# Kernel optimization log

Hardware: AMD Instinct MI355X
Metric: run time of the kernel (lower is better)

## Reference

```python
import jax, jax.numpy as jnp
import numpy as np

EPS = 1e-5  # InstanceNorm2d default eps


def setup_inputs() -> dict:
    key = jax.random.key(0)
    ks = jax.random.split(key, 5)
    B, T, C, N, H = 4, 8, 256, 196, 4
    s = 1.0 / np.sqrt(C)
    return {
        "emb": jax.random.normal(ks[0], (B, T, C, N), dtype=jnp.float32),
        "Wq": jax.random.normal(ks[1], (H, C, C), dtype=jnp.float32) * s,
        "Wk": jax.random.normal(ks[2], (H, C, C), dtype=jnp.float32) * s,
        "Wv": jax.random.normal(ks[3], (H, C, C), dtype=jnp.float32) * s,
        "Wo": jax.random.normal(ks[4], (C, C), dtype=jnp.float32) * s,
    }


def reference(emb, Wq, Wk, Wv, Wo):
    B, T, C, N = emb.shape
    S = T * N  # KV_size
    # emb.permute(0,1,3,2).view(B, T*N, C)
    x = jnp.transpose(emb, (0, 1, 3, 2)).reshape(B, S, C)
    # per-head full-width Linear projections (nn.Linear: y = x @ W.T)
    Q = jnp.einsum("bsc,hdc->bhsd", x, Wq)  # [B,H,S,C]
    K = jnp.einsum("bsc,hdc->bhsd", x, Wk)
    V = jnp.einsum("bsc,hdc->bhsd", x, Wv)
    scores = jnp.einsum("bhsd,bhtd->bhst", Q, K) / jnp.sqrt(jnp.float32(S))
    # InstanceNorm2d over each [S,S] map per (batch, head), no affine, biased var
    mean = jnp.mean(scores, axis=(-2, -1), keepdims=True)
    var = jnp.var(scores, axis=(-2, -1), keepdims=True)
    normed = (scores - mean) * jax.lax.rsqrt(var + EPS)
    probs = jax.nn.softmax(normed, axis=-1)  # attn_dropout: eval-mode identity
    ctx = jnp.einsum("bhst,bhtd->bhsd", probs, V)  # [B,H,S,C]
    ctx = jnp.mean(ctx, axis=1)  # mean over heads -> [B,S,C]
    O1 = jnp.einsum("bsc,dc->bsd", ctx, Wo)  # out Linear; proj_dropout identity
    # .view(-1, num_frames, num_channels, num_patches) on contiguous [B, T*N, C]
    return O1.reshape(B, T, C, N)
```

## Files before the change

kernel.cpp:

```cpp
#include <hip/hip_runtime.h>
#include <stdint.h>

typedef unsigned short u16;

#define Bb 4
#define Hh 4
#define Tt 8
#define Cc 256
#define NP 196
#define Ss 1568
#define SCALE_S 0.0252538136f

typedef __attribute__((ext_vector_type(4))) float floatx4;
typedef __attribute__((ext_vector_type(8))) short shortx8;

__device__ __forceinline__ float bf2f(u16 u) {
    union { unsigned u; float f; } v; v.u = ((unsigned)u) << 16; return v.f;
}
__device__ __forceinline__ u16 f2bf(float f) {
    union { float f; unsigned u; } v; v.f = f;
    unsigned r = v.u + 0x7FFFu + ((v.u >> 16) & 1u);
    return (u16)(r >> 16);
}

__global__ __launch_bounds__(256) void k_convw(const float* __restrict__ src, u16* __restrict__ dst, int n) {
    int i = blockIdx.x * 256 + threadIdx.x;
    if (i < n) dst[i] = f2bf(src[i]);
}

__device__ __forceinline__ void mfma_step(const u16* As, const u16* Bs, int lane,
                                          int wm, int wn, floatx4 acc[4][4]) {
    const int r15 = lane & 15;
    const int kq  = (lane >> 4) << 3;
    shortx8 a[4], b[4];
#pragma unroll
    for (int i = 0; i < 4; ++i)
        a[i] = *(const shortx8*)(As + (wm * 64 + i * 16 + r15) * 32 + kq);
#pragma unroll
    for (int j = 0; j < 4; ++j)
        b[j] = *(const shortx8*)(Bs + (wn * 64 + j * 16 + r15) * 32 + kq);
#pragma unroll
    for (int i = 0; i < 4; ++i)
#pragma unroll
        for (int j = 0; j < 4; ++j)
            acc[i][j] = __builtin_amdgcn_mfma_f32_16x16x32_bf16(a[i], b[j], acc[i][j], 0, 0, 0);
}

__device__ __forceinline__ void gemm_bt_core(const u16* A, const u16* Bm, int lda, int ldb,
                                             int mbase, int mlast, int nbase, int nlast,
                                             int KD, u16* As, u16* Bs, floatx4 acc[4][4]) {
    int tid = threadIdx.x;
    int lane = tid & 63, wave = tid >> 6, wm = wave >> 1, wn = wave & 1;
    int row0 = tid >> 2, row1 = 64 + (tid >> 2);
    int cole = (tid & 3) << 3;
    int ga0 = mbase + row0; ga0 = ga0 <= mlast ? ga0 : mlast;
    int ga1 = mbase + row1; ga1 = ga1 <= mlast ? ga1 : mlast;
    int gb0 = nbase + row0; gb0 = gb0 <= nlast ? gb0 : nlast;
    int gb1 = nbase + row1; gb1 = gb1 <= nlast ? gb1 : nlast;
    const u16* pa0 = A  + (size_t)ga0 * lda + cole;
    const u16* pa1 = A  + (size_t)ga1 * lda + cole;
    const u16* pb0 = Bm + (size_t)gb0 * ldb + cole;
    const u16* pb1 = Bm + (size_t)gb1 * ldb + cole;
    shortx8 va0 = *(const shortx8*)(pa0);
    shortx8 va1 = *(const shortx8*)(pa1);
    shortx8 vb0 = *(const shortx8*)(pb0);
    shortx8 vb1 = *(const shortx8*)(pb1);
    for (int k0 = 0; k0 < KD; k0 += 32) {
        __syncthreads();
        *(shortx8*)(As + row0 * 32 + cole) = va0;
        *(shortx8*)(As + row1 * 32 + cole) = va1;
        *(shortx8*)(Bs + row0 * 32 + cole) = vb0;
        *(shortx8*)(Bs + row1 * 32 + cole) = vb1;
        int k1 = k0 + 32;
        if (k1 < KD) {
            va0 = *(const shortx8*)(pa0 + k1);
            va1 = *(const shortx8*)(pa1 + k1);
            vb0 = *(const shortx8*)(pb0 + k1);
            vb1 = *(const shortx8*)(pb1 + k1);
        }
        __syncthreads();
        mfma_step(As, Bs, lane, wm, wn, acc);
    }
}

__global__ void k_transpose(const float* __restrict__ emb, u16* __restrict__ x) {
    __shared__ u16 tile[32][33];
    int bt = blockIdx.z;
    int c0 = blockIdx.y * 32, n0 = blockIdx.x * 32;
    const float* src = emb + (size_t)bt * Cc * NP;
#pragma unroll
    for (int rr = 0; rr < 32; rr += 8) {
        int c = c0 + threadIdx.y + rr;
        int n = n0 + threadIdx.x;
        u16 v = 0;
        if (n < NP) v = f2bf(src[(size_t)c * NP + n]);
        tile[threadIdx.y + rr][threadIdx.x] = v;
    }
    __syncthreads();
    int b = bt / Tt, t = bt % Tt;
    u16* dst = x + ((size_t)b * Ss + (size_t)t * NP) * Cc;
#pragma unroll
    for (int rr = 0; rr < 32; rr += 8) {
        int n = n0 + threadIdx.y + rr;
        int c = c0 + threadIdx.x;
        if (n < NP) dst[(size_t)n * Cc + c] = tile[threadIdx.x][threadIdx.y + rr];
    }
}

__global__ __launch_bounds__(256) void k_qkv(const u16* __restrict__ x,
                                             const u16* __restrict__ Wq,
                                             const u16* __restrict__ Wk,
                                             const u16* __restrict__ Wv,
                                             u16* __restrict__ Q, u16* __restrict__ Kb,
                                             u16* __restrict__ Vt) {
    __shared__ __align__(16) u16 As[128 * 32], Bs[128 * 32];
    floatx4 acc[4][4];
#pragma unroll
    for (int i = 0; i < 4; ++i)
#pragma unroll
        for (int j = 0; j < 4; ++j) acc[i][j] = (floatx4)(0.f);
    int z = blockIdx.z;
    int qkv = z >> 4, bh = z & 15, b = bh >> 2, h = bh & 3;
    const u16* A = x + (size_t)b * Ss * Cc;
    const u16* W = (qkv == 0 ? Wq : (qkv == 1 ? Wk : Wv)) + (size_t)h * Cc * Cc;
    int mbase = blockIdx.y * 128, nbase = blockIdx.x * 128;
    gemm_bt_core(A, W, Cc, Cc, mbase, Ss - 1, nbase, Cc - 1, Cc, As, Bs, acc);

    int tid = threadIdx.x, lane = tid & 63, wave = tid >> 6, wm = wave >> 1, wn = wave & 1;
    int rq = (lane >> 4) << 2, cn = lane & 15;
    if (qkv < 2) {
        u16* out = (qkv == 0 ? Q : Kb) + (size_t)bh * Ss * Cc;
#pragma unroll
        for (int i = 0; i < 4; ++i) {
            int mb = mbase + wm * 64 + i * 16 + rq;
#pragma unroll
            for (int j = 0; j < 4; ++j) {
                int n = nbase + wn * 64 + j * 16 + cn;
#pragma unroll
                for (int r = 0; r < 4; ++r) {
                    int m = mb + r;
                    if (m < Ss) out[(size_t)m * Cc + n] = f2bf(acc[i][j][r]);
                }
            }
        }
    } else {
        u16* out = Vt + (size_t)bh * Cc * Ss;
#pragma unroll
        for (int i = 0; i < 4; ++i) {
            int m0 = mbase + wm * 64 + i * 16 + rq;
            if (m0 < Ss) {
#pragma unroll
                for (int j = 0; j < 4; ++j) {
                    int n = nbase + wn * 64 + j * 16 + cn;
                    ushort4 v;
                    v.x = f2bf(acc[i][j][0]); v.y = f2bf(acc[i][j][1]);
                    v.z = f2bf(acc[i][j][2]); v.w = f2bf(acc[i][j][3]);
                    *(ushort4*)(out + (size_t)n * Ss + m0) = v;
                }
            }
        }
    }
}

__global__ __launch_bounds__(256) void k_scores(const u16* __restrict__ Q,
                                                const u16* __restrict__ Kb,
                                                u16* __restrict__ Sc, float* __restrict__ stats) {
    __shared__ __align__(16) u16 As[128 * 32], Bs[128 * 32];
    __shared__ float sred[8];
    floatx4 acc[4][4];
#pragma unroll
    for (int i = 0; i < 4; ++i)
#pragma unroll
        for (int j = 0; j < 4; ++j) acc[i][j] = (floatx4)(0.f);
    int bh = blockIdx.z;
    const u16* A  = Q  + (size_t)bh * Ss * Cc;
    const u16* Bm = Kb + (size_t)bh * Ss * Cc;
    int mbase = blockIdx.y * 128, nbase = blockIdx.x * 128;
    gemm_bt_core(A, Bm, Cc, Cc, mbase, Ss - 1, nbase, Ss - 1, Cc, As, Bs, acc);

    int tid = threadIdx.x, lane = tid & 63, wave = tid >> 6, wm = wave >> 1, wn = wave & 1;
    int rq = (lane >> 4) << 2, cn = lane & 15;
    u16* out = Sc + (size_t)bh * Ss * Ss;
    float lsum = 0.f, lsq = 0.f;
#pragma unroll
    for (int i = 0; i < 4; ++i) {
        int mb = mbase + wm * 64 + i * 16 + rq;
#pragma unroll
        for (int j = 0; j < 4; ++j) {
            int n = nbase + wn * 64 + j * 16 + cn;
            bool nv = n < Ss;
#pragma unroll
            for (int r = 0; r < 4; ++r) {
                int m = mb + r;
                if (nv && m < Ss) {
                    float v = acc[i][j][r] * SCALE_S;
                    out[(size_t)m * Ss + n] = f2bf(v);
                    lsum += v; lsq += v * v;
                }
            }
        }
    }
#pragma unroll
    for (int mk = 1; mk <= 32; mk <<= 1) { lsum += __shfl_xor(lsum, mk); lsq += __shfl_xor(lsq, mk); }
    if (lane == 0) { sred[wave] = lsum; sred[4 + wave] = lsq; }
    __syncthreads();
    if (tid == 0) atomicAdd(&stats[bh * 4 + 0], sred[0] + sred[1] + sred[2] + sred[3]);
    if (tid == 1) atomicAdd(&stats[bh * 4 + 1], sred[4] + sred[5] + sred[6] + sred[7]);
}

__global__ void k_stats(float* __restrict__ stats) {
    int i = threadIdx.x;
    if (i < 16) {
        float inv  = 1.f / ((float)Ss * (float)Ss);
        float mean = stats[i * 4] * inv;
        float var  = stats[i * 4 + 1] * inv - mean * mean;
        var = fmaxf(var, 0.f);
        stats[i * 4 + 2] = mean;
        stats[i * 4 + 3] = rsqrtf(var + 1e-5f);
    }
}

__global__ __launch_bounds__(256) void k_pv(const u16* __restrict__ Sc,
                                            const u16* __restrict__ Vt,
                                            const float* __restrict__ stats,
                                            float* __restrict__ ctxm) {
    __shared__ __align__(16) u16 As[128 * 32], Bs[128 * 32];
    __shared__ float rs[128];
    floatx4 acc[4][4];
#pragma unroll
    for (int i = 0; i < 4; ++i)
#pragma unroll
        for (int j = 0; j < 4; ++j) acc[i][j] = (floatx4)(0.f);
    int bh = blockIdx.z;
    float mean = stats[bh * 4 + 2], istd = stats[bh * 4 + 3];
    float aa = istd * 1.44269504f;
    float bb = -mean * aa;
    const u16* A  = Sc + (size_t)bh * Ss * Ss;
    const u16* Bm = Vt + (size_t)bh * Cc * Ss;
    int mbase = blockIdx.y * 128, nbase = blockIdx.x * 128;
    int tid = threadIdx.x, lane = tid & 63, wave = tid >> 6, wm = wave >> 1, wn = wave & 1;
    int row0 = tid >> 2, row1 = 64 + (tid >> 2);
    int cole = (tid & 3) << 3;
    int ga0 = mbase + row0; ga0 = ga0 <= Ss - 1 ? ga0 : Ss - 1;
    int ga1 = mbase + row1; ga1 = ga1 <= Ss - 1 ? ga1 : Ss - 1;
    const u16* pa0 = A + (size_t)ga0 * Ss + cole;
    const u16* pa1 = A + (size_t)ga1 * Ss + cole;
    const u16* pb0 = Bm + (size_t)(nbase + row0) * Ss + cole;
    const u16* pb1 = Bm + (size_t)(nbase + row1) * Ss + cole;
    float rsum0 = 0.f, rsum1 = 0.f;
    shortx8 v0 = *(const shortx8*)(pa0);
    shortx8 v1 = *(const shortx8*)(pa1);
    shortx8 vb0 = *(const shortx8*)(pb0);
    shortx8 vb1 = *(const shortx8*)(pb1);

    for (int k0 = 0; k0 < Ss; k0 += 32) {
        shortx8 o0, o1;
        float p0 = 0.f, p1 = 0.f;
#pragma unroll
        for (int e = 0; e < 8; ++e) {
            float f0 = bf2f((u16)v0[e]);
            float e0 = exp2f(f0 * aa + bb);
            p0 += e0; o0[e] = (short)f2bf(e0);
            float f1 = bf2f((u16)v1[e]);
            float e1 = exp2f(f1 * aa + bb);
            p1 += e1; o1[e] = (short)f2bf(e1);
        }
        rsum0 += p0; rsum1 += p1;
        __syncthreads();
        *(shortx8*)(As + row0 * 32 + cole) = o0;
        *(shortx8*)(As + row1 * 32 + cole) = o1;
        *(shortx8*)(Bs + row0 * 32 + cole) = vb0;
        *(shortx8*)(Bs + row1 * 32 + cole) = vb1;
        int k1 = k0 + 32;
        if (k1 < Ss) {
            v0  = *(const shortx8*)(pa0 + k1);
            v1  = *(const shortx8*)(pa1 + k1);
            vb0 = *(const shortx8*)(pb0 + k1);
            vb1 = *(const shortx8*)(pb1 + k1);
        }
        __syncthreads();
        mfma_step(As, Bs, lane, wm, wn, acc);
    }
    rsum0 += __shfl_xor(rsum0, 1); rsum0 += __shfl_xor(rsum0, 2);
    rsum1 += __shfl_xor(rsum1, 1); rsum1 += __shfl_xor(rsum1, 2);
    __syncthreads();
    if ((tid & 3) == 0) { rs[tid >> 2] = rsum0; rs[64 + (tid >> 2)] = rsum1; }
    __syncthreads();

    int b = bh >> 2;
    float* outp = ctxm + (size_t)b * Ss * Cc;
    int rq = (lane >> 4) << 2, cn = lane & 15;
#pragma unroll
    for (int i = 0; i < 4; ++i) {
        int ml = wm * 64 + i * 16 + rq;
#pragma unroll
        for (int r = 0; r < 4; ++r) {
            int m = mbase + ml + r;
            if (m < Ss) {
                float invs = 0.25f / rs[ml + r];
#pragma unroll
                for (int j = 0; j < 4; ++j) {
                    int n = nbase + wn * 64 + j * 16 + cn;
                    atomicAdd(&outp[(size_t)m * Cc + n], acc[i][j][r] * invs);
                }
            }
        }
    }
}

__global__ __launch_bounds__(256) void k_out(const float* __restrict__ ctxm,
                                             const u16* __restrict__ Wo, float* __restrict__ out) {
    __shared__ __align__(16) u16 As[128 * 32], Bs[128 * 32];
    floatx4 acc[4][4];
#pragma unroll
    for (int i = 0; i < 4; ++i)
#pragma unroll
        for (int j = 0; j < 4; ++j) acc[i][j] = (floatx4)(0.f);
    int b = blockIdx.z;
    const float* A = ctxm + (size_t)b * Ss * Cc;
    int mbase = blockIdx.y * 128, nbase = blockIdx.x * 128;
    int tid = threadIdx.x, lane = tid & 63, wave = tid >> 6, wm = wave >> 1, wn = wave & 1;
    int row0 = tid >> 2, row1 = 64 + (tid >> 2);
    int cole = (tid & 3) << 3;
    int ga0 = mbase + row0; ga0 = ga0 <= Ss - 1 ? ga0 : Ss - 1;
    int ga1 = mbase + row1; ga1 = ga1 <= Ss - 1 ? ga1 : Ss - 1;
    const float* pa0 = A + (size_t)ga0 * Cc + cole;
    const float* pa1 = A + (size_t)ga1 * Cc + cole;
    const u16* pb0 = Wo + (size_t)(nbase + row0 <= Cc - 1 ? nbase + row0 : Cc - 1) * Cc + cole;
    const u16* pb1 = Wo + (size_t)(nbase + row1 <= Cc - 1 ? nbase + row1 : Cc - 1) * Cc + cole;
    float4 a00 = *(const float4*)(pa0), a01 = *(const float4*)(pa0 + 4);
    float4 a10 = *(const float4*)(pa1), a11 = *(const float4*)(pa1 + 4);
    shortx8 vb0 = *(const shortx8*)(pb0);
    shortx8 vb1 = *(const shortx8*)(pb1);
    for (int k0 = 0; k0 < Cc; k0 += 32) {
        shortx8 o0, o1;
        o0[0] = (short)f2bf(a00.x); o0[1] = (short)f2bf(a00.y); o0[2] = (short)f2bf(a00.z); o0[3] = (short)f2bf(a00.w);
        o0[4] = (short)f2bf(a01.x); o0[5] = (short)f2bf(a01.y); o0[6] = (short)f2bf(a01.z); o0[7] = (short)f2bf(a01.w);
        o1[0] = (short)f2bf(a10.x); o1[1] = (short)f2bf(a10.y); o1[2] = (short)f2bf(a10.z); o1[3] = (short)f2bf(a10.w);
        o1[4] = (short)f2bf(a11.x); o1[5] = (short)f2bf(a11.y); o1[6] = (short)f2bf(a11.z); o1[7] = (short)f2bf(a11.w);
        __syncthreads();
        *(shortx8*)(As + row0 * 32 + cole) = o0;
        *(shortx8*)(As + row1 * 32 + cole) = o1;
        *(shortx8*)(Bs + row0 * 32 + cole) = vb0;
        *(shortx8*)(Bs + row1 * 32 + cole) = vb1;
        int k1 = k0 + 32;
        if (k1 < Cc) {
            a00 = *(const float4*)(pa0 + k1); a01 = *(const float4*)(pa0 + k1 + 4);
            a10 = *(const float4*)(pa1 + k1); a11 = *(const float4*)(pa1 + k1 + 4);
            vb0 = *(const shortx8*)(pb0 + k1);
            vb1 = *(const shortx8*)(pb1 + k1);
        }
        __syncthreads();
        mfma_step(As, Bs, lane, wm, wn, acc);
    }
    int rq = (lane >> 4) << 2, cn = lane & 15;
    float* o = out + (size_t)b * Ss * Cc;
#pragma unroll
    for (int i = 0; i < 4; ++i) {
        int mb = mbase + wm * 64 + i * 16 + rq;
#pragma unroll
        for (int j = 0; j < 4; ++j) {
            int n = nbase + wn * 64 + j * 16 + cn;
#pragma unroll
            for (int r = 0; r < 4; ++r) {
                int m = mb + r;
                if (m < Ss) o[(size_t)m * Cc + n] = acc[i][j][r];
            }
        }
    }
}

extern "C" void kernel_launch(void* const* d_in, const int* in_sizes, int n_in,
                              void* d_out, int out_size, void* d_ws, size_t ws_size,
                              hipStream_t stream) {
    const float* emb = (const float*)d_in[0];
    float* out = (float*)d_out;

    char* ws = (char*)d_ws;
    size_t off = 0;
    auto alloc = [&](size_t bytes) -> void* {
        void* p = ws + off;
        off = (off + bytes + 255) & ~(size_t)255;
        return p;
    };
    float* stats = (float*)alloc(16 * 4 * sizeof(float));
    u16* Wqc  = (u16*)alloc((size_t)Hh * Cc * Cc * 2);
    u16* Wkc  = (u16*)alloc((size_t)Hh * Cc * Cc * 2);
    u16* Wvc  = (u16*)alloc((size_t)Hh * Cc * Cc * 2);
    u16* Woc  = (u16*)alloc((size_t)Cc * Cc * 2);
    u16* x    = (u16*)alloc((size_t)Bb * Ss * Cc * 2);
    u16* Q    = (u16*)alloc((size_t)Bb * Hh * Ss * Cc * 2);
    u16* Kb   = (u16*)alloc((size_t)Bb * Hh * Ss * Cc * 2);
    u16* Vt   = (u16*)alloc((size_t)Bb * Hh * Ss * Cc * 2);
    float* ctxm = (float*)alloc((size_t)Bb * Ss * Cc * 4);
    u16* Sc   = (u16*)alloc((size_t)Bb * Hh * Ss * Ss * 2);

    hipMemsetAsync(stats, 0, 16 * 4 * sizeof(float), stream);
    hipMemsetAsync(ctxm, 0, (size_t)Bb * Ss * Cc * 4, stream);

    k_convw<<<dim3(1024), dim3(256), 0, stream>>>((const float*)d_in[1], Wqc, Hh * Cc * Cc);
    k_convw<<<dim3(1024), dim3(256), 0, stream>>>((const float*)d_in[2], Wkc, Hh * Cc * Cc);
    k_convw<<<dim3(1024), dim3(256), 0, stream>>>((const float*)d_in[3], Wvc, Hh * Cc * Cc);
    k_convw<<<dim3(256),  dim3(256), 0, stream>>>((const float*)d_in[4], Woc, Cc * Cc);

    k_transpose<<<dim3(7, 8, 32), dim3(32, 8), 0, stream>>>(emb, x);
    k_qkv<<<dim3(2, 13, 48), dim3(256), 0, stream>>>(x, Wqc, Wkc, Wvc, Q, Kb, Vt);
    k_scores<<<dim3(13, 13, 16), dim3(256), 0, stream>>>(Q, Kb, Sc, stats);
    k_stats<<<dim3(1), dim3(64), 0, stream>>>(stats);
    k_pv<<<dim3(2, 13, 16), dim3(256), 0, stream>>>(Sc, Vt, stats, ctxm);
    k_out<<<dim3(2, 13, 4), dim3(256), 0, stream>>>(ctxm, Woc, out);
}
```

Baseline: 255.1 us.

## Split PV over the key dimension with a separate row-sum pass

Softmax row sums move into a new k_rowsum kernel, so the PV kernel no longer needs the whole key range per block. k_pv now uses 64x256 output tiles that cover the full channel width, which means each score tile is exponentiated once instead of twice. The key dimension is split four ways across blocks, raising the grid from 416 to 1600 blocks. In exchange the score matrix is read one extra time by the row-sum pass, and atomic adds into ctxm grow with the split-K partials.

New measurement: 328.4 us. 28.7% more time.

```diff
diff --git a/kernel.cpp b/kernel.cpp
--- a/kernel.cpp
+++ b/kernel.cpp
@@ -220,87 +220,105 @@
     }
 }
 
+__global__ __launch_bounds__(256) void k_rowsum(const u16* __restrict__ Sc,
+                                                const float* __restrict__ stats,
+                                                float* __restrict__ rowsums) {
+    __shared__ float red[4];
+    int s = blockIdx.x, bh = blockIdx.y;
+    int tid = threadIdx.x, lane = tid & 63, wave = tid >> 6;
+    float istd = stats[bh * 4 + 3];
+    float aa = istd * 1.44269504f;
+    float bb = -stats[bh * 4 + 2] * aa;
+    const u16* srow = Sc + ((size_t)bh * Ss + s) * Ss;
+    float part = 0.f;
+#pragma unroll
+    for (int rep = 0; rep < 7; ++rep) {
+        int t = tid + rep * 256;
+        if (t < Ss) part += exp2f(bf2f(srow[t]) * aa + bb);
+    }
+#pragma unroll
+    for (int mk = 1; mk <= 32; mk <<= 1) part += __shfl_xor(part, mk);
+    if (lane == 0) red[wave] = part;
+    __syncthreads();
+    if (tid == 0) rowsums[(size_t)bh * Ss + s] = red[0] + red[1] + red[2] + red[3];
+}
+
 __global__ __launch_bounds__(256) void k_pv(const u16* __restrict__ Sc,
                                             const u16* __restrict__ Vt,
                                             const float* __restrict__ stats,
+                                            const float* __restrict__ rowsums,
                                             float* __restrict__ ctxm) {
-    __shared__ __align__(16) u16 As[128 * 32], Bs[128 * 32];
-    __shared__ float rs[128];
+    __shared__ __align__(16) u16 As[64 * 32], Bs[256 * 32];
     floatx4 acc[4][4];
 #pragma unroll
     for (int i = 0; i < 4; ++i)
 #pragma unroll
         for (int j = 0; j < 4; ++j) acc[i][j] = (floatx4)(0.f);
-    int bh = blockIdx.z;
-    float mean = stats[bh * 4 + 2], istd = stats[bh * 4 + 3];
+    int z = blockIdx.z;
+    int bh = z >> 2, split = z & 3;
+    int mbase = blockIdx.x * 64;
+    float istd = stats[bh * 4 + 3];
     float aa = istd * 1.44269504f;
-    float bb = -mean * aa;
+    float bb = -stats[bh * 4 + 2] * aa;
     const u16* A  = Sc + (size_t)bh * Ss * Ss;
     const u16* Bm = Vt + (size_t)bh * Cc * Ss;
-    int mbase = blockIdx.y * 128, nbase = blockIdx.x * 128;
-    int tid = threadIdx.x, lane = tid & 63, wave = tid >> 6, wm = wave >> 1, wn = wave & 1;
-    int row0 = tid >> 2, row1 = 64 + (tid >> 2);
+    int tid = threadIdx.x, lane = tid & 63, wave = tid >> 6;
+    int row  = tid >> 2;
     int cole = (tid & 3) << 3;
-    int ga0 = mbase + row0; ga0 = ga0 <= Ss - 1 ? ga0 : Ss - 1;
-    int ga1 = mbase + row1; ga1 = ga1 <= Ss - 1 ? ga1 : Ss - 1;
-    const u16* pa0 = A + (size_t)ga0 * Ss + cole;
-    const u16* pa1 = A + (size_t)ga1 * Ss + cole;
-    const u16* pb0 = Bm + (size_t)(nbase + row0) * Ss + cole;
-    const u16* pb1 = Bm + (size_t)(nbase + row1) * Ss + cole;
-    float rsum0 = 0.f, rsum1 = 0.f;
-    shortx8 v0 = *(const shortx8*)(pa0);
-    shortx8 v1 = *(const shortx8*)(pa1);
-    shortx8 vb0 = *(const shortx8*)(pb0);
-    shortx8 vb1 = *(const shortx8*)(pb1);
-
-    for (int k0 = 0; k0 < Ss; k0 += 32) {
-        shortx8 o0, o1;
-        float p0 = 0.f, p1 = 0.f;
+    int ga = mbase + row; ga = ga <= Ss - 1 ? ga : Ss - 1;
+    const u16* pa = A + (size_t)ga * Ss + cole;
+    const u16* pb0 = Bm + (size_t)(row)       * Ss + cole;
+    const u16* pb1 = Bm + (size_t)(row + 64)  * Ss + cole;
+    const u16* pb2 = Bm + (size_t)(row + 128) * Ss + cole;
+    const u16* pb3 = Bm + (size_t)(row + 192) * Ss + cole;
+    int t0 = ((49 * split) / 4) * 32;
+    int t1 = ((49 * (split + 1)) / 4) * 32;
+    shortx8 va  = *(const shortx8*)(pa + t0);
+    shortx8 vb0 = *(const shortx8*)(pb0 + t0);
+    shortx8 vb1 = *(const shortx8*)(pb1 + t0);
+    shortx8 vb2 = *(const shortx8*)(pb2 + t0);
+    shortx8 vb3 = *(const shortx8*)(pb3 + t0);
+
+    for (int k0 = t0; k0 < t1; k0 += 32) {
+        shortx8 o;
 #pragma unroll
         for (int e = 0; e < 8; ++e) {
-            float f0 = bf2f((u16)v0[e]);
-            float e0 = exp2f(f0 * aa + bb);
-            p0 += e0; o0[e] = (short)f2bf(e0);
-            float f1 = bf2f((u16)v1[e]);
-            float e1 = exp2f(f1 * aa + bb);
-            p1 += e1; o1[e] = (short)f2bf(e1);
-        }
-        rsum0 += p0; rsum1 += p1;
-        __syncthreads();
-        *(shortx8*)(As + row0 * 32 + cole) = o0;
-        *(shortx8*)(As + row1 * 32 + cole) = o1;
-        *(shortx8*)(Bs + row0 * 32 + cole) = vb0;
-        *(shortx8*)(Bs + row1 * 32 + cole) = vb1;
+            float f = bf2f((u16)va[e]);
+            o[e] = (short)f2bf(exp2f(f * aa + bb));
+        }
+        __syncthreads();
+        *(shortx8*)(As + row * 32 + cole) = o;
+        *(shortx8*)(Bs + (row)       * 32 + cole) = vb0;
+        *(shortx8*)(Bs + (row + 64)  * 32 + cole) = vb1;
+        *(shortx8*)(Bs + (row + 128) * 32 + cole) = vb2;
+        *(shortx8*)(Bs + (row + 192) * 32 + cole) = vb3;
         int k1 = k0 + 32;
-        if (k1 < Ss) {
-            v0  = *(const shortx8*)(pa0 + k1);
-            v1  = *(const shortx8*)(pa1 + k1);
+        if (k1 < t1) {
+            va  = *(const shortx8*)(pa + k1);
             vb0 = *(const shortx8*)(pb0 + k1);
             vb1 = *(const shortx8*)(pb1 + k1);
-        }
-        __syncthreads();
-        mfma_step(As, Bs, lane, wm, wn, acc);
-    }
-    rsum0 += __shfl_xor(rsum0, 1); rsum0 += __shfl_xor(rsum0, 2);
-    rsum1 += __shfl_xor(rsum1, 1); rsum1 += __shfl_xor(rsum1, 2);
-    __syncthreads();
-    if ((tid & 3) == 0) { rs[tid >> 2] = rsum0; rs[64 + (tid >> 2)] = rsum1; }
-    __syncthreads();
+            vb2 = *(const shortx8*)(pb2 + k1);
+            vb3 = *(const shortx8*)(pb3 + k1);
+        }
+        __syncthreads();
+        mfma_step(As, Bs, lane, 0, wave, acc);
+    }
 
     int b = bh >> 2;
     float* outp = ctxm + (size_t)b * Ss * Cc;
+    const float* rsb = rowsums + (size_t)bh * Ss;
     int rq = (lane >> 4) << 2, cn = lane & 15;
 #pragma unroll
     for (int i = 0; i < 4; ++i) {
-        int ml = wm * 64 + i * 16 + rq;
+        int ml = i * 16 + rq;
 #pragma unroll
         for (int r = 0; r < 4; ++r) {
             int m = mbase + ml + r;
             if (m < Ss) {
-                float invs = 0.25f / rs[ml + r];
+                float invs = 0.25f / rsb[m];
 #pragma unroll
                 for (int j = 0; j < 4; ++j) {
-                    int n = nbase + wn * 64 + j * 16 + cn;
+                    int n = wave * 64 + j * 16 + cn;
                     atomicAdd(&outp[(size_t)m * Cc + n], acc[i][j][r] * invs);
                 }
             }
@@ -384,6 +402,7 @@
         return p;
     };
     float* stats = (float*)alloc(16 * 4 * sizeof(float));
+    float* rowsums = (float*)alloc((size_t)16 * Ss * sizeof(float));
     u16* Wqc  = (u16*)alloc((size_t)Hh * Cc * Cc * 2);
     u16* Wkc  = (u16*)alloc((size_t)Hh * Cc * Cc * 2);
     u16* Wvc  = (u16*)alloc((size_t)Hh * Cc * Cc * 2);
@@ -407,6 +426,7 @@
     k_qkv<<<dim3(2, 13, 48), dim3(256), 0, stream>>>(x, Wqc, Wkc, Wvc, Q, Kb, Vt);
     k_scores<<<dim3(13, 13, 16), dim3(256), 0, stream>>>(Q, Kb, Sc, stats);
     k_stats<<<dim3(1), dim3(64), 0, stream>>>(stats);
-    k_pv<<<dim3(2, 13, 16), dim3(256), 0, stream>>>(Sc, Vt, stats, ctxm);
+    k_rowsum<<<dim3(Ss, 16), dim3(256), 0, stream>>>(Sc, stats, rowsums);
+    k_pv<<<dim3(25, 1, 64), dim3(256), 0, stream>>>(Sc, Vt, stats, rowsums, ctxm);
     k_out<<<dim3(2, 13, 4), dim3(256), 0, stream>>>(ctxm, Woc, out);
 }
```
